# Kernel optimization log

Measured on AMD Instinct MI355X. Metric: run time of the kernel, lower is better.

## Reference

```python
import jax, jax.numpy as jnp
import numpy as np

N_JOINTS = 24
JOINT_TREES = np.array([0,0,0,0,1,2,3,4,5,6,7,8,9,9,9,12,13,14,16,17,18,19,20,21])

def _build_adj():
    adj = np.eye(N_JOINTS, dtype=np.float32)
    for i, j in enumerate(JOINT_TREES):
        if i == j:
            continue
        adj[j, i] = 1.0
        adj[i, j] = 1.0
    return adj

ADJ = jnp.asarray(_build_adj())            # [N, N], with self-loops (diag=1)
MASK = jnp.ones((1, N_JOINTS, 1), jnp.float32).at[:, 0, :].set(0.0)  # root_id=0 masked

DIMS = [13, 64, 64, 64, 65]  # per_node_input -> W -> W -> W -> output_ch


def setup_inputs() -> dict:
    key = jax.random.key(0)
    ks = jax.random.split(key, 1 + 3 * 4)
    B = 65536
    inp = {"x": jax.random.normal(ks[0], (B, N_JOINTS, DIMS[0]), jnp.float32)}
    ki = 1
    for i in range(4):
        fan_in = DIMS[i]
        bound = 1.0 / np.sqrt(fan_in)
        # per-node weights (ParallelLinear, bias=False inside DensePNGCN)
        inp[f"w{i}"] = jax.random.uniform(ks[ki], (N_JOINTS, DIMS[i], DIMS[i + 1]), jnp.float32, -bound, bound); ki += 1
        # learnable adjacency weights: ~init 0.05 +- 0.05, diag forced to 1
        aw = jnp.clip(0.05 + (jax.random.uniform(ks[ki], (N_JOINTS, N_JOINTS)) - 0.5) * 0.1, 0.01, 1.0)
        aw = aw.at[jnp.arange(N_JOINTS), jnp.arange(N_JOINTS)].set(1.0)
        inp[f"aw{i}"] = aw.astype(jnp.float32); ki += 1
        # DenseWGCN bias (init zeros; random here for a non-trivial baseline)
        inp[f"b{i}"] = jax.random.normal(ks[ki], (DIMS[i + 1],), jnp.float32) * 0.01; ki += 1
    return inp


def reference(x, w0, w1, w2, w3, aw0, aw1, aw2, aw3, b0, b1, b2, b3):
    ws = [w0, w1, w2, w3]
    aws = [aw0, aw1, aw2, aw3]
    bs = [b0, b1, b2, b3]
    n = x * MASK  # mask_root: zero out root joint input
    n_layers = len(ws)
    for i in range(n_layers):
        # per-node linear (ParallelLinear, no bias)
        h = jnp.einsum('bkl,klj->bkj', n, ws[i])
        # dense weighted adjacency aggregation
        adj_w = aws[i] * ADJ  # [N, N]
        h = jnp.einsum('nm,bmj->bnj', adj_w, h)
        n = h + bs[i]
        if i + 1 < n_layers:
            n = jax.nn.relu(n)
    return n
```

## Files before the change

### kernel.cpp

```cpp
#include <hip/hip_runtime.h>


#define NJ 24
#define TB 16
#define STR 72

typedef __attribute__((ext_vector_type(8))) short bf16x8;
typedef __attribute__((ext_vector_type(4))) float f32x4;

__device__ constexpr int NBR_OFF_C[NJ + 1] = {0,4,7,10,13,16,19,22,25,28,33,35,37,40,43,46,48,51,54,57,60,63,66,68,70};
__device__ constexpr int NBR_LIST_C[70] = {
    0,1,2,3,  0,1,4,  0,2,5,  0,3,6,  1,4,7,  2,5,8,  3,6,9,  4,7,10,
    5,8,11,  6,9,12,13,14,  7,10,  8,11,  9,12,15,  9,13,16,  9,14,17,
    12,15,  13,16,18,  14,17,19,  16,18,20,  17,19,21,  18,20,22,  19,21,23,
    20,22,  21,23
};

__device__ __forceinline__ float bf2f(unsigned short u) {
    return __uint_as_float(((unsigned int)u) << 16);
}
__device__ __forceinline__ unsigned short f2bf(float f) {
    unsigned int u = __float_as_uint(f);
    u += 0x7fffu + ((u >> 16) & 1u);
    return (unsigned short)(u >> 16);
}
__device__ __forceinline__ unsigned int pack2(float a, float b) {
    return (unsigned int)f2bf(a) | ((unsigned int)f2bf(b) << 16);
}

__global__ __launch_bounds__(256) void prepack(
    const float* __restrict__ w0, const float* __restrict__ w1,
    const float* __restrict__ w2, const float* __restrict__ w3,
    unsigned short* __restrict__ wp)
{
    const int f = blockIdx.x;
    const int t = threadIdx.x;
    const int lane = t >> 2;
    const int jp = t & 3;

    const float* w; int DIN, DOUT, joint, mt, kt;
    if (f < 96)       { w = w0; DIN = 13; DOUT = 64; int g = f;       joint = g >> 2; mt = g & 3;        kt = 0;     }
    else if (f < 288) { w = w1; DIN = 64; DOUT = 64; int g = f - 96;  joint = g >> 3; mt = (g >> 1) & 3; kt = g & 1; }
    else if (f < 480) { w = w2; DIN = 64; DOUT = 64; int g = f - 288; joint = g >> 3; mt = (g >> 1) & 3; kt = g & 1; }
    else              { w = w3; DIN = 64; DOUT = 65; int g = f - 480; joint = g / 10; int r = g % 10; mt = r >> 1; kt = r & 1; }

    const int jout = mt * 16 + (lane & 15);
    unsigned int packed = 0;
#pragma unroll
    for (int jj = 0; jj < 2; ++jj) {
        const int j = jp * 2 + jj;
        const int l = kt * 32 + (lane >> 4) * 8 + j;
        float v = 0.f;
        if (l < DIN && jout < DOUT) v = w[(joint * DIN + l) * DOUT + jout];
        packed |= (unsigned int)f2bf(v) << (16 * jj);
    }
    *(unsigned int*)(wp + (size_t)f * 512 + lane * 8 + jp * 2) = packed;
}

template<int KT, int MT>
__device__ __forceinline__ void linear_phase(unsigned short* buf,
    const unsigned short* __restrict__ wf, int wv, int lane)
{
    const int bl = lane & 15;
    const int quad = lane >> 4;
    for (int jj = 0; jj < 6; ++jj) {
        const int k = wv * 6 + jj;
        bf16x8 bfr[KT];
#pragma unroll
        for (int kt = 0; kt < KT; ++kt)
            bfr[kt] = *(bf16x8*)&buf[(k * TB + bl) * STR + kt * 32 + quad * 8];
        const unsigned short* wj = wf + (size_t)k * (MT * KT * 512) + lane * 8;
        bf16x8 afr[MT][KT];
#pragma unroll
        for (int mt = 0; mt < MT; ++mt)
#pragma unroll
            for (int kt = 0; kt < KT; ++kt)
                afr[mt][kt] = *(const bf16x8*)(wj + (mt * KT + kt) * 512);
        f32x4 acc[MT];
#pragma unroll
        for (int mt = 0; mt < MT; ++mt) {
            acc[mt] = (f32x4){0.f, 0.f, 0.f, 0.f};
#pragma unroll
            for (int kt = 0; kt < KT; ++kt)
                acc[mt] = __builtin_amdgcn_mfma_f32_16x16x32_bf16(afr[mt][kt], bfr[kt], acc[mt], 0, 0, 0);
        }
#pragma unroll
        for (int mt = 0; mt < MT; ++mt) {
            if (mt < 4 || quad == 0) {
                uint2 p;
                p.x = pack2(acc[mt].x, acc[mt].y);
                p.y = pack2(acc[mt].z, acc[mt].w);
                *(uint2*)&buf[(k * TB + bl) * STR + mt * 16 + quad * 4] = p;
            }
        }
    }
}

template<bool LAST>
__device__ __forceinline__ void agg_phase(unsigned short* buf,
    const float* __restrict__ aw, const float* __restrict__ bias,
    float* __restrict__ out, int base, int wv, int lane)
{
    const int bsub = lane >> 4;
    const int jq = lane & 15;
    const int b = wv * 4 + bsub;

    float acc[NJ][4];
#pragma unroll
    for (int n = 0; n < NJ; ++n) {
        acc[n][0] = 0.f; acc[n][1] = 0.f; acc[n][2] = 0.f; acc[n][3] = 0.f;
    }
    const float4 bv = *(const float4*)(bias + jq * 4);

#pragma unroll
    for (int m = 0; m < NJ; ++m) {
        uint2 raw = *(uint2*)&buf[(m * TB + b) * STR + jq * 4];
        const float h0 = __uint_as_float(raw.x << 16);
        const float h1 = __uint_as_float(raw.x & 0xffff0000u);
        const float h2 = __uint_as_float(raw.y << 16);
        const float h3 = __uint_as_float(raw.y & 0xffff0000u);
#pragma unroll
        for (int e = NBR_OFF_C[m]; e < NBR_OFF_C[m + 1]; ++e) {
            const int n = NBR_LIST_C[e];
            const float c = aw[n * NJ + m];
            acc[n][0] += c * h0; acc[n][1] += c * h1;
            acc[n][2] += c * h2; acc[n][3] += c * h3;
        }
    }

    if (!LAST) {
#pragma unroll
        for (int n = 0; n < NJ; ++n) {
            const float v0 = fmaxf(acc[n][0] + bv.x, 0.f);
            const float v1 = fmaxf(acc[n][1] + bv.y, 0.f);
            const float v2 = fmaxf(acc[n][2] + bv.z, 0.f);
            const float v3 = fmaxf(acc[n][3] + bv.w, 0.f);
            uint2 p; p.x = pack2(v0, v1); p.y = pack2(v2, v3);
            *(uint2*)&buf[(n * TB + b) * STR + jq * 4] = p;
        }
    } else {
        float* ob = out + (size_t)(base + b) * (NJ * 65);
#pragma unroll
        for (int n = 0; n < NJ; ++n) {
            float* p = ob + n * 65 + jq * 4;
            p[0] = acc[n][0] + bv.x;
            p[1] = acc[n][1] + bv.y;
            p[2] = acc[n][2] + bv.z;
            p[3] = acc[n][3] + bv.w;
        }
        if (lane < NJ) {
            const int n = lane;
            float a64[4] = {0.f, 0.f, 0.f, 0.f};
            for (int e = NBR_OFF_C[n]; e < NBR_OFF_C[n + 1]; ++e) {
                const int m = NBR_LIST_C[e];
                const float c = aw[n * NJ + m];
#pragma unroll
                for (int bb = 0; bb < 4; ++bb)
                    a64[bb] += c * bf2f(buf[(m * TB + wv * 4 + bb) * STR + 64]);
            }
            const float b64v = bias[64];
#pragma unroll
            for (int bb = 0; bb < 4; ++bb)
                out[(size_t)(base + wv * 4 + bb) * (NJ * 65) + n * 65 + 64] = a64[bb] + b64v;
        }
    }
}

__global__ __launch_bounds__(256, 2) void gnn_mfma(
    const float* __restrict__ x, const unsigned short* __restrict__ wp,
    const float* __restrict__ aw0, const float* __restrict__ b0,
    const float* __restrict__ aw1, const float* __restrict__ b1,
    const float* __restrict__ aw2, const float* __restrict__ b2,
    const float* __restrict__ aw3, const float* __restrict__ b3,
    float* __restrict__ out)
{
    __shared__ __align__(16) unsigned short buf[NJ * TB * STR];

    const int t = threadIdx.x;
    const int lane = t & 63;
    const int wv = t >> 6;
    const int base = blockIdx.x * TB;

    for (int i = t; i < NJ * TB * 16; i += 256) {
        const int k = i >> 8;
        const int b = (i >> 4) & 15;
        const int f2 = (i & 15) * 2;
        float v0 = 0.f, v1 = 0.f;
        if (k > 0) {
            const float* xr = x + (size_t)(base + b) * 312 + k * 13;
            if (f2 < 13)     v0 = xr[f2];
            if (f2 + 1 < 13) v1 = xr[f2 + 1];
        }
        *(unsigned int*)&buf[(k * TB + b) * STR + f2] = pack2(v0, v1);
    }
    __syncthreads();

    linear_phase<1, 4>(buf, wp, wv, lane);
    __syncthreads();
    agg_phase<false>(buf, aw0, b0, nullptr, base, wv, lane);
    __syncthreads();
    linear_phase<2, 4>(buf, wp + 96 * 512, wv, lane);
    __syncthreads();
    agg_phase<false>(buf, aw1, b1, nullptr, base, wv, lane);
    __syncthreads();
    linear_phase<2, 4>(buf, wp + 288 * 512, wv, lane);
    __syncthreads();
    agg_phase<false>(buf, aw2, b2, nullptr, base, wv, lane);
    __syncthreads();
    linear_phase<2, 5>(buf, wp + 480 * 512, wv, lane);
    __syncthreads();
    agg_phase<true>(buf, aw3, b3, out, base, wv, lane);
}

extern "C" void kernel_launch(void* const* d_in, const int* in_sizes, int n_in,
                              void* d_out, int out_size, void* d_ws, size_t ws_size,
                              hipStream_t stream)
{
    const float* x   = (const float*)d_in[0];
    const float* w0  = (const float*)d_in[1];
    const float* aw0 = (const float*)d_in[2];
    const float* b0  = (const float*)d_in[3];
    const float* w1  = (const float*)d_in[4];
    const float* aw1 = (const float*)d_in[5];
    const float* b1  = (const float*)d_in[6];
    const float* w2  = (const float*)d_in[7];
    const float* aw2 = (const float*)d_in[8];
    const float* b2  = (const float*)d_in[9];
    const float* w3  = (const float*)d_in[10];
    const float* aw3 = (const float*)d_in[11];
    const float* b3  = (const float*)d_in[12];
    float* out = (float*)d_out;
    unsigned short* wp = (unsigned short*)d_ws;

    prepack<<<720, 256, 0, stream>>>(w0, w1, w2, w3, wp);

    const int blocks = 65536 / TB;
    gnn_mfma<<<blocks, 256, 0, stream>>>(x, wp, aw0, b0, aw1, b1,
                                         aw2, b2, aw3, b3, out);
}
```

Before: 795.9 us.

## Replace padded LDS rows with XOR swizzle and split 65th output column

Shrinks each activation row in shared memory from a padded stride of 72 to 64 elements and uses an XOR swizzle on the column index to avoid bank conflicts. The extra 65th output channel of the last layer moves into a small separate LDS array. Its aggregation is now computed by the jq==0 lanes inside the main output loop instead of a separate lane<24 pass. The smaller LDS footprint lets launch bounds ask for 3 blocks per CU instead of 2, at the risk of register pressure or spills from the 96-float accumulator array.

```diff
diff --git a/kernel.cpp b/kernel.cpp
--- a/kernel.cpp
+++ b/kernel.cpp
@@ -3,7 +3,6 @@
 
 #define NJ 24
 #define TB 16
-#define STR 72
 
 typedef __attribute__((ext_vector_type(8))) short bf16x8;
 typedef __attribute__((ext_vector_type(4))) float f32x4;
@@ -58,17 +57,19 @@
 }
 
 template<int KT, int MT>
-__device__ __forceinline__ void linear_phase(unsigned short* buf,
+__device__ __forceinline__ void linear_phase(unsigned short* buf, unsigned short* abuf,
     const unsigned short* __restrict__ wf, int wv, int lane)
 {
     const int bl = lane & 15;
     const int quad = lane >> 4;
+    const int sx = (bl & 7) << 3;
     for (int jj = 0; jj < 6; ++jj) {
         const int k = wv * 6 + jj;
+        const int rbase = (k * TB + bl) * 64;
         bf16x8 bfr[KT];
 #pragma unroll
         for (int kt = 0; kt < KT; ++kt)
-            bfr[kt] = *(bf16x8*)&buf[(k * TB + bl) * STR + kt * 32 + quad * 8];
+            bfr[kt] = *(bf16x8*)&buf[rbase + ((kt * 32 + quad * 8) ^ sx)];
         const unsigned short* wj = wf + (size_t)k * (MT * KT * 512) + lane * 8;
         bf16x8 afr[MT][KT];
 #pragma unroll
@@ -86,11 +87,13 @@
         }
 #pragma unroll
         for (int mt = 0; mt < MT; ++mt) {
-            if (mt < 4 || quad == 0) {
+            if (mt < 4) {
                 uint2 p;
                 p.x = pack2(acc[mt].x, acc[mt].y);
                 p.y = pack2(acc[mt].z, acc[mt].w);
-                *(uint2*)&buf[(k * TB + bl) * STR + mt * 16 + quad * 4] = p;
+                *(uint2*)&buf[rbase + ((mt * 16 + quad * 4) ^ sx)] = p;
+            } else if (quad == 0) {
+                abuf[k * TB + bl] = f2bf(acc[mt].x);
             }
         }
     }
@@ -98,12 +101,14 @@
 
 template<bool LAST>
 __device__ __forceinline__ void agg_phase(unsigned short* buf,
+    const unsigned short* abuf,
     const float* __restrict__ aw, const float* __restrict__ bias,
     float* __restrict__ out, int base, int wv, int lane)
 {
     const int bsub = lane >> 4;
     const int jq = lane & 15;
     const int b = wv * 4 + bsub;
+    const int eo = (jq * 4) ^ ((b & 7) << 3);
 
     float acc[NJ][4];
 #pragma unroll
@@ -114,7 +119,7 @@
 
 #pragma unroll
     for (int m = 0; m < NJ; ++m) {
-        uint2 raw = *(uint2*)&buf[(m * TB + b) * STR + jq * 4];
+        uint2 raw = *(uint2*)&buf[(m * TB + b) * 64 + eo];
         const float h0 = __uint_as_float(raw.x << 16);
         const float h1 = __uint_as_float(raw.x & 0xffff0000u);
         const float h2 = __uint_as_float(raw.y << 16);
@@ -136,9 +141,10 @@
             const float v2 = fmaxf(acc[n][2] + bv.z, 0.f);
             const float v3 = fmaxf(acc[n][3] + bv.w, 0.f);
             uint2 p; p.x = pack2(v0, v1); p.y = pack2(v2, v3);
-            *(uint2*)&buf[(n * TB + b) * STR + jq * 4] = p;
+            *(uint2*)&buf[(n * TB + b) * 64 + eo] = p;
         }
     } else {
+        const float b64v = bias[64];
         float* ob = out + (size_t)(base + b) * (NJ * 65);
 #pragma unroll
         for (int n = 0; n < NJ; ++n) {
@@ -147,26 +153,20 @@
             p[1] = acc[n][1] + bv.y;
             p[2] = acc[n][2] + bv.z;
             p[3] = acc[n][3] + bv.w;
-        }
-        if (lane < NJ) {
-            const int n = lane;
-            float a64[4] = {0.f, 0.f, 0.f, 0.f};
-            for (int e = NBR_OFF_C[n]; e < NBR_OFF_C[n + 1]; ++e) {
-                const int m = NBR_LIST_C[e];
-                const float c = aw[n * NJ + m];
-#pragma unroll
-                for (int bb = 0; bb < 4; ++bb)
-                    a64[bb] += c * bf2f(buf[(m * TB + wv * 4 + bb) * STR + 64]);
+            if (jq == 0) {
+                float s = b64v;
+#pragma unroll
+                for (int e = NBR_OFF_C[n]; e < NBR_OFF_C[n + 1]; ++e) {
+                    const int m = NBR_LIST_C[e];
+                    s += aw[n * NJ + m] * bf2f(abuf[m * TB + b]);
+                }
+                p[64] = s;
             }
-            const float b64v = bias[64];
-#pragma unroll
-            for (int bb = 0; bb < 4; ++bb)
-                out[(size_t)(base + wv * 4 + bb) * (NJ * 65) + n * 65 + 64] = a64[bb] + b64v;
-        }
-    }
-}
-
-__global__ __launch_bounds__(256, 2) void gnn_mfma(
+        }
+    }
+}
+
+__global__ __launch_bounds__(256, 3) void gnn_mfma(
     const float* __restrict__ x, const unsigned short* __restrict__ wp,
     const float* __restrict__ aw0, const float* __restrict__ b0,
     const float* __restrict__ aw1, const float* __restrict__ b1,
@@ -174,7 +174,8 @@
     const float* __restrict__ aw3, const float* __restrict__ b3,
     float* __restrict__ out)
 {
-    __shared__ __align__(16) unsigned short buf[NJ * TB * STR];
+    __shared__ __align__(16) unsigned short buf[NJ * TB * 64];
+    __shared__ __align__(8)  unsigned short abuf[NJ * TB];
 
     const int t = threadIdx.x;
     const int lane = t & 63;
@@ -191,25 +192,26 @@
             if (f2 < 13)     v0 = xr[f2];
             if (f2 + 1 < 13) v1 = xr[f2 + 1];
         }
-        *(unsigned int*)&buf[(k * TB + b) * STR + f2] = pack2(v0, v1);
-    }
-    __syncthreads();
-
-    linear_phase<1, 4>(buf, wp, wv, lane);
-    __syncthreads();
-    agg_phase<false>(buf, aw0, b0, nullptr, base, wv, lane);
-    __syncthreads();
-    linear_phase<2, 4>(buf, wp + 96 * 512, wv, lane);
-    __syncthreads();
-    agg_phase<false>(buf, aw1, b1, nullptr, base, wv, lane);
-    __syncthreads();
-    linear_phase<2, 4>(buf, wp + 288 * 512, wv, lane);
-    __syncthreads();
-    agg_phase<false>(buf, aw2, b2, nullptr, base, wv, lane);
-    __syncthreads();
-    linear_phase<2, 5>(buf, wp + 480 * 512, wv, lane);
-    __syncthreads();
-    agg_phase<true>(buf, aw3, b3, out, base, wv, lane);
+        const int row = k * TB + b;
+        *(unsigned int*)&buf[row * 64 + (f2 ^ ((row & 7) << 3))] = pack2(v0, v1);
+    }
+    __syncthreads();
+
+    linear_phase<1, 4>(buf, abuf, wp, wv, lane);
+    __syncthreads();
+    agg_phase<false>(buf, abuf, aw0, b0, nullptr, base, wv, lane);
+    __syncthreads();
+    linear_phase<2, 4>(buf, abuf, wp + 96 * 512, wv, lane);
+    __syncthreads();
+    agg_phase<false>(buf, abuf, aw1, b1, nullptr, base, wv, lane);
+    __syncthreads();
+    linear_phase<2, 4>(buf, abuf, wp + 288 * 512, wv, lane);
+    __syncthreads();
+    agg_phase<false>(buf, abuf, aw2, b2, nullptr, base, wv, lane);
+    __syncthreads();
+    linear_phase<2, 5>(buf, abuf, wp + 480 * 512, wv, lane);
+    __syncthreads();
+    agg_phase<true>(buf, abuf, aw3, b3, out, base, wv, lane);
 }
 
 extern "C" void kernel_launch(void* const* d_in, const int* in_sizes, int n_in,
```

New measurement: 746.0 us. 6.3% less time.
